# Optimization experiments

Measured on AMD Instinct MI355X. Metric: run time of the kernel, lower is better.

The kernel has to match this reference:

```python
import jax, jax.numpy as jnp
import numpy as np

N = 100_000      # nodes
E = 1_600_000    # edges
NG = 512         # graphs in batch
EPS = 1e-5


def _prop(x, src, dst, n, add_self_loops):
    """GCN-normalized sparse propagation: agg_i = sum_{j->i} d_j^-1/2 d_i^-1/2 x_j."""
    ones = jnp.ones(src.shape[0], x.dtype)
    deg = jax.ops.segment_sum(ones, dst, num_segments=n)
    if add_self_loops:
        deg = deg + 1.0
    dinv = jnp.where(deg > 0, jax.lax.rsqrt(jnp.maximum(deg, 1e-12)), 0.0)
    w = dinv[src] * dinv[dst]                       # [E]
    agg = jax.ops.segment_sum(x[src] * w[:, None], dst, num_segments=n)
    if add_self_loops:
        agg = agg + x * (dinv * dinv)[:, None]
    return agg


def setup_inputs() -> dict:
    key = jax.random.key(0)
    ks = jax.random.split(key, 24)
    w = lambda k, s: jax.random.normal(k, s, jnp.float32) * 0.05
    dim = 100
    return {
        "x": jax.random.normal(ks[0], (N, 128), jnp.float32),
        "src": jax.random.randint(ks[1], (E,), 0, N),
        "dst": jax.random.randint(ks[2], (E,), 0, N),
        "batch": jnp.sort(jax.random.randint(ks[3], (N,), 0, NG)),
        # SGConv 1 & 2 (propagate then Linear)
        "W1": w(ks[4], (128, dim)), "b1": jnp.zeros((dim,), jnp.float32),
        "W2": w(ks[5], (dim, dim)), "b2": jnp.zeros((dim,), jnp.float32),
        # BatchNorm1d affine params
        "gamma": jnp.ones((dim,), jnp.float32), "beta": jnp.zeros((dim,), jnp.float32),
        # ARMAConv (num_stacks=1, num_layers=1)
        "Wa_init": w(ks[6], (dim, dim)), "Wa_root": w(ks[7], (dim, dim)),
        "ba": jnp.zeros((dim,), jnp.float32),
        # MLP head
        "Wf1": w(ks[8], (dim, 2 * dim)), "bf1": jnp.zeros((2 * dim,), jnp.float32),
        "Wf2": w(ks[9], (2 * dim, 3 * dim)), "bf2": jnp.zeros((3 * dim,), jnp.float32),
        "Wf3": w(ks[10], (3 * dim, 2 * dim)), "bf3": jnp.zeros((2 * dim,), jnp.float32),
        "Wf4": w(ks[11], (2 * dim, 1)), "bf4": jnp.zeros((1,), jnp.float32),
    }


def reference(x, src, dst, batch, W1, b1, W2, b2, gamma, beta,
              Wa_init, Wa_root, ba, Wf1, bf1, Wf2, bf2, Wf3, bf3, Wf4, bf4):
    n = x.shape[0]
    # SGConv (K=1): propagate with self-loop gcn_norm, then linear; ReLU
    h = jax.nn.relu(_prop(x, src, dst, n, True) @ W1 + b1)
    h = jax.nn.relu(_prop(h, src, dst, n, True) @ W2 + b2)
    # BatchNorm1d (training mode: batch statistics, biased var)
    mu = jnp.mean(h, axis=0)
    var = jnp.mean((h - mu) ** 2, axis=0)
    h = (h - mu) * jax.lax.rsqrt(var + EPS) * gamma + beta
    # ARMAConv (1 stack, 1 layer): ReLU(A_hat (h W_init) + h W_root + b), no self-loops
    a = jax.nn.relu(_prop(h @ Wa_init, src, dst, n, False) + h @ Wa_root + ba)
    # global_add_pool over graph ids
    g = jax.ops.segment_sum(a, batch, num_segments=NG)   # [NG, dim]
    # MLP head
    g = jax.nn.relu(g @ Wf1 + bf1)
    g = jax.nn.relu(g @ Wf2 + bf2)
    g = jax.nn.relu(g @ Wf3 + bf3)
    return g @ Wf4 + bf4
```

## Files before the change

kernel.cpp:

```cpp
#include <hip/hip_runtime.h>
#include <hip/hip_fp16.h>

#define NNODES 100000
#define NEDGES 1600000
#define NGRAPH 512
#define DIM    100
#define DP     128
#define EPSBN  1e-5f
#define NBUK   ((NNODES + 255) >> 8)
#define BINCH  8192

typedef _Float16 half8 __attribute__((ext_vector_type(8)));
typedef float floatx4 __attribute__((ext_vector_type(4)));

__global__ __launch_bounds__(256) void bin_count_kernel(const int* __restrict__ dst,
                                                        int* __restrict__ btotal, int e) {
    __shared__ int lc[NBUK];
    int tid = threadIdx.x;
    int base = blockIdx.x * BINCH;
    int m = e - base; if (m > BINCH) m = BINCH;
    for (int b = tid; b < NBUK; b += 256) lc[b] = 0;
    __syncthreads();
    for (int j = tid; j < m; j += 256)
        atomicAdd(&lc[dst[base + j] >> 8], 1);
    __syncthreads();
    for (int b = tid; b < NBUK; b += 256)
        if (lc[b]) atomicAdd(&btotal[b], lc[b]);
}

__global__ void bucket_scan_kernel(const int* __restrict__ btotal, int* __restrict__ bbase,
                                   int* __restrict__ bcursor, int e) {
    __shared__ int s[512];
    int tid = threadIdx.x;
    int v = (tid < NBUK) ? btotal[tid] : 0;
    s[tid] = v; __syncthreads();
    for (int o = 1; o < 512; o <<= 1) {
        int t = (tid >= o) ? s[tid - o] : 0;
        __syncthreads();
        s[tid] += t;
        __syncthreads();
    }
    if (tid < NBUK) {
        int base = s[tid] - v;
        bbase[tid] = base;
        bcursor[tid] = base;
    }
    if (tid == 0) bbase[NBUK] = e;
}

__global__ __launch_bounds__(256) void bin_kernel(
        const int* __restrict__ src, const int* __restrict__ dst,
        int* __restrict__ bcursor, int2* __restrict__ gpairs, int e) {
    __shared__ int2 lpairs[BINCH];
    __shared__ int lcount[NBUK], lstart[NBUK], lcur[NBUK], gbase[NBUK];
    int tid = threadIdx.x;
    int base = blockIdx.x * BINCH;
    int m = e - base; if (m > BINCH) m = BINCH;

    for (int b = tid; b < NBUK; b += 256) lcount[b] = 0;
    __syncthreads();
    for (int j = tid; j < m; j += 256)
        atomicAdd(&lcount[dst[base + j] >> 8], 1);
    __syncthreads();
    if (tid == 0) {
        int acc = 0;
        for (int b = 0; b < NBUK; b++) {
            lstart[b] = acc;
            lcur[b] = acc;
            acc += lcount[b];
        }
    }
    __syncthreads();
    for (int b = tid; b < NBUK; b += 256)
        gbase[b] = atomicAdd(&bcursor[b], lcount[b]);
    for (int j = tid; j < m; j += 256) {
        int s = src[base + j], d = dst[base + j];
        int p = atomicAdd(&lcur[d >> 8], 1);
        lpairs[p] = make_int2(s, d);
    }
    __syncthreads();
    for (int j = tid; j < m; j += 256) {
        int2 pr = lpairs[j];
        int b = pr.y >> 8;
        gpairs[gbase[b] + (j - lstart[b])] = pr;
    }
}

__global__ __launch_bounds__(256) void bucket_build_kernel(
        const int2* __restrict__ gpairs, const int* __restrict__ bbase,
        int* __restrict__ off, int* __restrict__ ssorted,
        float* __restrict__ dsl, float* __restrict__ dnsl, int n, int e) {
    __shared__ int cnt[256];
    __shared__ int sc[256];
    int b = blockIdx.x, tid = threadIdx.x;
    int node0 = b << 8;
    int e0 = bbase[b], e1 = bbase[b + 1];

    cnt[tid] = 0;
    __syncthreads();
    for (int j = e0 + tid; j < e1; j += 256)
        atomicAdd(&cnt[gpairs[j].y & 255], 1);
    __syncthreads();

    int c = cnt[tid];
    sc[tid] = c; __syncthreads();
    for (int o = 1; o < 256; o <<= 1) {
        int t = (tid >= o) ? sc[tid - o] : 0;
        __syncthreads();
        sc[tid] += t;
        __syncthreads();
    }
    int excl = sc[tid] - c;

    int node = node0 + tid;
    if (node < n) {
        off[node] = e0 + excl;
        float cf = (float)c;
        dsl[node] = rsqrtf(cf + 1.0f);
        dnsl[node] = (c > 0) ? rsqrtf(cf) : 0.0f;
    }
    if (b == NBUK - 1 && tid == 0) off[n] = e;

    __syncthreads();
    cnt[tid] = e0 + excl;
    __syncthreads();
    for (int j = e0 + tid; j < e1; j += 256) {
        int2 pr = gpairs[j];
        int p = atomicAdd(&cnt[pr.y & 255], 1);
        ssorted[p] = pr.x;
    }
}

__global__ void packW4_kernel(const float* __restrict__ W1, const float* __restrict__ W2,
                              const float* __restrict__ W3, const float* __restrict__ W4,
                              _Float16* __restrict__ Wt1, _Float16* __restrict__ Wt2,
                              _Float16* __restrict__ Wt3, _Float16* __restrict__ Wt4) {
    int which = blockIdx.x >> 6;
    int idx = (blockIdx.x & 63) * 256 + threadIdx.x;
    const float* W = (which == 0) ? W1 : (which == 1) ? W2 : (which == 2) ? W3 : W4;
    _Float16* Wt  = (which == 0) ? Wt1 : (which == 1) ? Wt2 : (which == 2) ? Wt3 : Wt4;
    int K = (which == 0) ? 128 : DIM;
    int j = idx & 7;
    int l = (idx >> 3) & 63;
    int c = idx >> 9;
    int t = c >> 2, k0 = c & 3;
    int nn = t * 16 + (l & 15);
    int k = k0 * 32 + (l >> 4) * 8 + j;
    float v = (k < K && nn < DIM) ? W[k * DIM + nn] : 0.f;
    Wt[idx] = (_Float16)v;
}

__global__ void padb_kernel(const float* __restrict__ b1, const float* __restrict__ b2,
                            float* __restrict__ b1p, float* __restrict__ b2p) {
    int c = threadIdx.x;
    b1p[c] = (c < DIM) ? b1[c] : 0.f;
    b2p[c] = (c < DIM) ? b2[c] : 0.f;
}

__global__ __launch_bounds__(256) void prop_kernel(
        const __half* __restrict__ pre, const int* __restrict__ ssorted,
        const int* __restrict__ off, const float* __restrict__ dinv,
        const float* __restrict__ bias, __half* __restrict__ outH, int n) {
    int wave = (blockIdx.x * blockDim.x + threadIdx.x) >> 6;
    int lane = threadIdx.x & 63;
    if (wave >= n) return;
    int e0 = off[wave], e1 = off[wave + 1];
    int deg = e1 - e0;
    int g = lane >> 4;
    int q = lane & 15;

    float acc[8];
#pragma unroll
    for (int i = 0; i < 8; i++) acc[i] = 0.f;

    auto addu = [&](uint4 u) {
        float2 f;
        f = __half22float2(*(__half2*)&u.x); acc[0] += f.x; acc[1] += f.y;
        f = __half22float2(*(__half2*)&u.y); acc[2] += f.x; acc[3] += f.y;
        f = __half22float2(*(__half2*)&u.z); acc[4] += f.x; acc[5] += f.y;
        f = __half22float2(*(__half2*)&u.w); acc[6] += f.x; acc[7] += f.y;
    };
    auto rowptr = [&](int s) -> const uint4* {
        return (const uint4*)&pre[(long)s * DP + q * 8];
    };

    for (int base = 0; base < deg; base += 64) {
        int m = deg - base; if (m > 64) m = 64;
        int sidx = (lane < m) ? ssorted[e0 + base + lane] : 0;
        int j = 0;
        for (; j + 16 <= m; j += 16) {
            int s0 = __shfl(sidx, j + g);
            int s1 = __shfl(sidx, j + 4 + g);
            int s2 = __shfl(sidx, j + 8 + g);
            int s3 = __shfl(sidx, j + 12 + g);
            uint4 u0 = *rowptr(s0);
            uint4 u1 = *rowptr(s1);
            uint4 u2 = *rowptr(s2);
            uint4 u3 = *rowptr(s3);
            addu(u0); addu(u1); addu(u2); addu(u3);
        }
        for (; j + 4 <= m; j += 4) {
            int s = __shfl(sidx, j + g);
            addu(*rowptr(s));
        }
        if (j < m) {
            int r = m - j;
            int s = __shfl(sidx, (g < r) ? j + g : j);
            if (g < r) addu(*rowptr(s));
        }
    }

#pragma unroll
    for (int i = 0; i < 8; i++) {
        acc[i] += __shfl_xor(acc[i], 16);
        acc[i] += __shfl_xor(acc[i], 32);
    }

    if (g == 0) {
        float dn = dinv[wave];
        addu(*rowptr(wave));
        float4 b0 = *(const float4*)&bias[q * 8];
        float4 b1v = *(const float4*)&bias[q * 8 + 4];
        float o[8];
        o[0] = fmaxf(dn * acc[0] + b0.x, 0.f);
        o[1] = fmaxf(dn * acc[1] + b0.y, 0.f);
        o[2] = fmaxf(dn * acc[2] + b0.z, 0.f);
        o[3] = fmaxf(dn * acc[3] + b0.w, 0.f);
        o[4] = fmaxf(dn * acc[4] + b1v.x, 0.f);
        o[5] = fmaxf(dn * acc[5] + b1v.y, 0.f);
        o[6] = fmaxf(dn * acc[6] + b1v.z, 0.f);
        o[7] = fmaxf(dn * acc[7] + b1v.w, 0.f);
        __half2 p0 = __floats2half2_rn(o[0], o[1]);
        __half2 p1 = __floats2half2_rn(o[2], o[3]);
        __half2 p2 = __floats2half2_rn(o[4], o[5]);
        __half2 p3 = __floats2half2_rn(o[6], o[7]);
        uint4 u;
        u.x = *(unsigned int*)&p0;
        u.y = *(unsigned int*)&p1;
        u.z = *(unsigned int*)&p2;
        u.w = *(unsigned int*)&p3;
        *(uint4*)&outH[(long)wave * DP + q * 8] = u;
    }
}

__global__ __launch_bounds__(256) void prop_arma_kernel(
        const __half* __restrict__ pre, const int* __restrict__ ssorted,
        const int* __restrict__ off, const float* __restrict__ dinv,
        const __half* __restrict__ R, __half* __restrict__ outH, int n) {
    int wave = (blockIdx.x * blockDim.x + threadIdx.x) >> 6;
    int lane = threadIdx.x & 63;
    if (wave >= n) return;
    int e0 = off[wave], e1 = off[wave + 1];
    int deg = e1 - e0;
    int g = lane >> 4;
    int q = lane & 15;

    float acc[8];
#pragma unroll
    for (int i = 0; i < 8; i++) acc[i] = 0.f;

    auto addu = [&](uint4 u) {
        float2 f;
        f = __half22float2(*(__half2*)&u.x); acc[0] += f.x; acc[1] += f.y;
        f = __half22float2(*(__half2*)&u.y); acc[2] += f.x; acc[3] += f.y;
        f = __half22float2(*(__half2*)&u.z); acc[4] += f.x; acc[5] += f.y;
        f = __half22float2(*(__half2*)&u.w); acc[6] += f.x; acc[7] += f.y;
    };
    auto rowptr = [&](int s) -> const uint4* {
        return (const uint4*)&pre[(long)s * DP + q * 8];
    };

    for (int base = 0; base < deg; base += 64) {
        int m = deg - base; if (m > 64) m = 64;
        int sidx = (lane < m) ? ssorted[e0 + base + lane] : 0;
        int j = 0;
        for (; j + 16 <= m; j += 16) {
            int s0 = __shfl(sidx, j + g);
            int s1 = __shfl(sidx, j + 4 + g);
            int s2 = __shfl(sidx, j + 8 + g);
            int s3 = __shfl(sidx, j + 12 + g);
            uint4 u0 = *rowptr(s0);
            uint4 u1 = *rowptr(s1);
            uint4 u2 = *rowptr(s2);
            uint4 u3 = *rowptr(s3);
            addu(u0); addu(u1); addu(u2); addu(u3);
        }
        for (; j + 4 <= m; j += 4) {
            int s = __shfl(sidx, j + g);
            addu(*rowptr(s));
        }
        if (j < m) {
            int r = m - j;
            int s = __shfl(sidx, (g < r) ? j + g : j);
            if (g < r) addu(*rowptr(s));
        }
    }

#pragma unroll
    for (int i = 0; i < 8; i++) {
        acc[i] += __shfl_xor(acc[i], 16);
        acc[i] += __shfl_xor(acc[i], 32);
    }

    if (g == 0) {
        float dn = dinv[wave];
        uint4 r4 = *(const uint4*)&R[(long)wave * DP + q * 8];
        float rr[8];
        float2 f;
        f = __half22float2(*(__half2*)&r4.x); rr[0] = f.x; rr[1] = f.y;
        f = __half22float2(*(__half2*)&r4.y); rr[2] = f.x; rr[3] = f.y;
        f = __half22float2(*(__half2*)&r4.z); rr[4] = f.x; rr[5] = f.y;
        f = __half22float2(*(__half2*)&r4.w); rr[6] = f.x; rr[7] = f.y;
        float o[8];
#pragma unroll
        for (int i = 0; i < 8; i++) o[i] = fmaxf(dn * acc[i] + rr[i], 0.f);
        __half2 p0 = __floats2half2_rn(o[0], o[1]);
        __half2 p1 = __floats2half2_rn(o[2], o[3]);
        __half2 p2 = __floats2half2_rn(o[4], o[5]);
        __half2 p3 = __floats2half2_rn(o[6], o[7]);
        uint4 u;
        u.x = *(unsigned int*)&p0;
        u.y = *(unsigned int*)&p1;
        u.z = *(unsigned int*)&p2;
        u.w = *(unsigned int*)&p3;
        *(uint4*)&outH[(long)wave * DP + q * 8] = u;
    }
}

__global__ __launch_bounds__(256) void matmul_a32_kernel(
        const float* __restrict__ A, const _Float16* __restrict__ WtF,
        const float* __restrict__ rowscale, __half* __restrict__ Ch, int M) {
    __shared__ char smraw[64 * 132 * 4];
    _Float16* Bs = (_Float16*)smraw;
    float* Ct = (float*)smraw;
    int tid = threadIdx.x;
    int wave = tid >> 6;
    int lane = tid & 63;
    int m16 = lane & 15;
    int quad = lane >> 4;
    long row0blk = (long)blockIdx.x * 64;
    long row0 = row0blk + wave * 16;

    {
        const uint4* s = (const uint4*)WtF;
        uint4* d = (uint4*)Bs;
        for (int i = tid; i < 2048; i += 256) d[i] = s[i];
    }

    half8 af[4];
    {
        long ar = row0 + m16; if (ar >= M) ar = M - 1;
        const float* Ap = &A[ar * DP + quad * 8];
#pragma unroll
        for (int k0 = 0; k0 < 4; k0++) {
            float4 v0 = *(const float4*)(Ap + k0 * 32);
            float4 v1 = *(const float4*)(Ap + k0 * 32 + 4);
            half8 o;
            o[0] = (_Float16)v0.x; o[1] = (_Float16)v0.y;
            o[2] = (_Float16)v0.z; o[3] = (_Float16)v0.w;
            o[4] = (_Float16)v1.x; o[5] = (_Float16)v1.y;
            o[6] = (_Float16)v1.z; o[7] = (_Float16)v1.w;
            af[k0] = o;
        }
    }
    __syncthreads();

    floatx4 acc[8];
#pragma unroll
    for (int t = 0; t < 8; t++) acc[t] = (floatx4){0.f, 0.f, 0.f, 0.f};

#pragma unroll
    for (int c = 0; c < 32; c++) {
        half8 bf = *(const half8*)&Bs[(c * 64 + lane) * 8];
        acc[c >> 2] = __builtin_amdgcn_mfma_f32_16x16x32_f16(af[c & 3], bf, acc[c >> 2], 0, 0, 0);
    }
    __syncthreads();

    int lrow0 = wave * 16 + quad * 4;
#pragma unroll
    for (int t = 0; t < 8; t++)
#pragma unroll
        for (int r = 0; r < 4; r++)
            Ct[(lrow0 + r) * 132 + t * 16 + m16] = acc[t][r];
    __syncthreads();

    for (int idx = tid; idx < 64 * 32; idx += 256) {
        int lr = idx >> 5, c4 = idx & 31;
        long grow = row0blk + lr;
        if (grow >= M) continue;
        int col = c4 * 4;
        float4 v = *(const float4*)&Ct[lr * 132 + col];
        float rs = rowscale[grow];
        v.x *= rs; v.y *= rs; v.z *= rs; v.w *= rs;
        __half2 p01 = __floats2half2_rn(v.x, v.y);
        __half2 p23 = __floats2half2_rn(v.z, v.w);
        uint2 u;
        u.x = *(unsigned int*)&p01;
        u.y = *(unsigned int*)&p23;
        *(uint2*)&Ch[grow * DP + col] = u;
    }
}

__global__ __launch_bounds__(256) void matmul_a16_kernel(
        const __half* __restrict__ A, const _Float16* __restrict__ WtF,
        const float* __restrict__ rowscale, __half* __restrict__ Ch, int M) {
    __shared__ char smraw[64 * 132 * 4];
    _Float16* Bs = (_Float16*)smraw;
    float* Ct = (float*)smraw;
    int tid = threadIdx.x;
    int wave = tid >> 6;
    int lane = tid & 63;
    int m16 = lane & 15;
    int quad = lane >> 4;
    long row0blk = (long)blockIdx.x * 64;
    long row0 = row0blk + wave * 16;

    {
        const uint4* s = (const uint4*)WtF;
        uint4* d = (uint4*)Bs;
        for (int i = tid; i < 2048; i += 256) d[i] = s[i];
    }

    half8 af[4];
    {
        long ar = row0 + m16; if (ar >= M) ar = M - 1;
        const _Float16* Ap = (const _Float16*)&A[ar * DP + quad * 8];
#pragma unroll
        for (int k0 = 0; k0 < 4; k0++)
            af[k0] = *(const half8*)(Ap + k0 * 32);
    }
    __syncthreads();

    floatx4 acc[8];
#pragma unroll
    for (int t = 0; t < 8; t++) acc[t] = (floatx4){0.f, 0.f, 0.f, 0.f};

#pragma unroll
    for (int c = 0; c < 32; c++) {
        half8 bf = *(const half8*)&Bs[(c * 64 + lane) * 8];
        acc[c >> 2] = __builtin_amdgcn_mfma_f32_16x16x32_f16(af[c & 3], bf, acc[c >> 2], 0, 0, 0);
    }
    __syncthreads();

    int lrow0 = wave * 16 + quad * 4;
#pragma unroll
    for (int t = 0; t < 8; t++)
#pragma unroll
        for (int r = 0; r < 4; r++)
            Ct[(lrow0 + r) * 132 + t * 16 + m16] = acc[t][r];
    __syncthreads();

    for (int idx = tid; idx < 64 * 32; idx += 256) {
        int lr = idx >> 5, c4 = idx & 31;
        long grow = row0blk + lr;
        if (grow >= M) continue;
        int col = c4 * 4;
        float4 v = *(const float4*)&Ct[lr * 132 + col];
        float rs = rowscale[grow];
        v.x *= rs; v.y *= rs; v.z *= rs; v.w *= rs;
        __half2 p01 = __floats2half2_rn(v.x, v.y);
        __half2 p23 = __floats2half2_rn(v.z, v.w);
        uint2 u;
        u.x = *(unsigned int*)&p01;
        u.y = *(unsigned int*)&p23;
        *(uint2*)&Ch[grow * DP + col] = u;
    }
}

__global__ __launch_bounds__(256) void matmul_dual_kernel(
        const __half* __restrict__ A, const _Float16* __restrict__ WtF3,
        const _Float16* __restrict__ WtF4, const float* __restrict__ ba,
        const float* __restrict__ rowscale,
        const float* __restrict__ bnscale, const float* __restrict__ bnshift,
        __half* __restrict__ Ch1, __half* __restrict__ ChR, int M, int Kout) {
    __shared__ char smraw[64 * 132 * 4];
    _Float16* Bs = (_Float16*)smraw;
    float* Ct = (float*)smraw;
    int tid = threadIdx.x;
    int wave = tid >> 6;
    int lane = tid & 63;
    int m16 = lane & 15;
    int quad = lane >> 4;
    long row0blk = (long)blockIdx.x * 64;
    long row0 = row0blk + wave * 16;

    half8 af[4];
    {
        long ar = row0 + m16; if (ar >= M) ar = M - 1;
        const _Float16* Ap = (const _Float16*)&A[ar * DP + quad * 8];
#pragma unroll
        for (int k0 = 0; k0 < 4; k0++) {
            half8 h = *(const half8*)(Ap + k0 * 32);
            int c0 = quad * 8 + k0 * 32;
            float4 sc0 = *(const float4*)&bnscale[c0];
            float4 sc1 = *(const float4*)&bnscale[c0 + 4];
            float4 sh0 = *(const float4*)&bnshift[c0];
            float4 sh1 = *(const float4*)&bnshift[c0 + 4];
            half8 o;
            o[0] = (_Float16)((float)h[0] * sc0.x + sh0.x);
            o[1] = (_Float16)((float)h[1] * sc0.y + sh0.y);
            o[2] = (_Float16)((float)h[2] * sc0.z + sh0.z);
            o[3] = (_Float16)((float)h[3] * sc0.w + sh0.w);
            o[4] = (_Float16)((float)h[4] * sc1.x + sh1.x);
            o[5] = (_Float16)((float)h[5] * sc1.y + sh1.y);
            o[6] = (_Float16)((float)h[6] * sc1.z + sh1.z);
            o[7] = (_Float16)((float)h[7] * sc1.w + sh1.w);
            af[k0] = o;
        }
    }

    floatx4 acc3[8], acc4[8];
#pragma unroll
    for (int t = 0; t < 8; t++) {
        acc3[t] = (floatx4){0.f, 0.f, 0.f, 0.f};
        acc4[t] = (floatx4){0.f, 0.f, 0.f, 0.f};
    }

    {
        const uint4* s = (const uint4*)WtF3;
        uint4* d = (uint4*)Bs;
        for (int i = tid; i < 2048; i += 256) d[i] = s[i];
    }
    __syncthreads();
#pragma unroll
    for (int c = 0; c < 32; c++) {
        half8 bf = *(const half8*)&Bs[(c * 64 + lane) * 8];
        acc3[c >> 2] = __builtin_amdgcn_mfma_f32_16x16x32_f16(af[c & 3], bf, acc3[c >> 2], 0, 0, 0);
    }
    __syncthreads();

    {
        const uint4* s = (const uint4*)WtF4;
        uint4* d = (uint4*)Bs;
        for (int i = tid; i < 2048; i += 256) d[i] = s[i];
    }
    __syncthreads();
#pragma unroll
    for (int c = 0; c < 32; c++) {
        half8 bf = *(const half8*)&Bs[(c * 64 + lane) * 8];
        acc4[c >> 2] = __builtin_amdgcn_mfma_f32_16x16x32_f16(af[c & 3], bf, acc4[c >> 2], 0, 0, 0);
    }
    __syncthreads();

    int lrow0 = wave * 16 + quad * 4;

#pragma unroll
    for (int t = 0; t < 8; t++)
#pragma unroll
        for (int r = 0; r < 4; r++)
            Ct[(lrow0 + r) * 132 + t * 16 + m16] = acc3[t][r];
    __syncthreads();
    for (int idx = tid; idx < 64 * 32; idx += 256) {
        int lr = idx >> 5, c4 = idx & 31;
        long grow = row0blk + lr;
        if (grow >= M) continue;
        int col = c4 * 4;
        float4 v = *(const float4*)&Ct[lr * 132 + col];
        float rs = rowscale[grow];
        v.x *= rs; v.y *= rs; v.z *= rs; v.w *= rs;
        __half2 p01 = __floats2half2_rn(v.x, v.y);
        __half2 p23 = __floats2half2_rn(v.z, v.w);
        uint2 u;
        u.x = *(unsigned int*)&p01;
        u.y = *(unsigned int*)&p23;
        *(uint2*)&Ch1[grow * DP + col] = u;
    }
    __syncthreads();

#pragma unroll
    for (int t = 0; t < 8; t++)
#pragma unroll
        for (int r = 0; r < 4; r++)
            Ct[(lrow0 + r) * 132 + t * 16 + m16] = acc4[t][r];
    __syncthreads();
    for (int idx = tid; idx < 64 * 32; idx += 256) {
        int lr = idx >> 5, c4 = idx & 31;
        long grow = row0blk + lr;
        if (grow >= M) continue;
        int col = c4 * 4;
        float4 v = *(const float4*)&Ct[lr * 132 + col];
        if (col + 4 <= Kout) {
            float4 bb = *(const float4*)&ba[col];
            v.x += bb.x; v.y += bb.y; v.z += bb.z; v.w += bb.w;
        }
        __half2 p01 = __floats2half2_rn(v.x, v.y);
        __half2 p23 = __floats2half2_rn(v.z, v.w);
        uint2 u;
        u.x = *(unsigned int*)&p01;
        u.y = *(unsigned int*)&p23;
        *(uint2*)&ChR[grow * DP + col] = u;
    }
}

__global__ __launch_bounds__(512) void bnstats_kernel(const __half* __restrict__ h,
                                                      float* __restrict__ bnsum,
                                                      float* __restrict__ bnsq, int n) {
    __shared__ float2 sred[512], qred[512];
    int tid = threadIdx.x;
    int col2 = tid & 63;
    int rgrp = tid >> 6;
    float2 s = make_float2(0.f, 0.f), qv = make_float2(0.f, 0.f);
    if (col2 < 52) {
        for (int r = blockIdx.x * 8 + rgrp; r < n; r += gridDim.x * 8) {
            __half2 hv = *(const __half2*)&h[(long)r * DP + col2 * 2];
            float2 f = __half22float2(hv);
            s.x += f.x; s.y += f.y;
            qv.x += f.x * f.x; qv.y += f.y * f.y;
        }
    }
    sred[tid] = s; qred[tid] = qv;
    __syncthreads();
    if (tid < 52) {
        float2 ts = make_float2(0.f, 0.f), tq = make_float2(0.f, 0.f);
#pragma unroll
        for (int gg = 0; gg < 8; gg++) {
            float2 v = sred[gg * 64 + tid]; ts.x += v.x; ts.y += v.y;
            v = qred[gg * 64 + tid]; tq.x += v.x; tq.y += v.y;
        }
        atomicAdd(&bnsum[tid * 2], ts.x);
        atomicAdd(&bnsum[tid * 2 + 1], ts.y);
        atomicAdd(&bnsq[tid * 2], tq.x);
        atomicAdd(&bnsq[tid * 2 + 1], tq.y);
    }
}

__global__ void bn_prep_kernel(const float* __restrict__ sum, const float* __restrict__ sq,
                               const float* __restrict__ gamma, const float* __restrict__ beta,
                               float* __restrict__ scale, float* __restrict__ shift, int n) {
    int c = threadIdx.x;
    float sc = 0.f, sh = 0.f;
    if (c < DIM) {
        float inv_n = 1.0f / (float)n;
        float mu = sum[c] * inv_n;
        float var = sq[c] * inv_n - mu * mu;
        float rs = rsqrtf(var + EPSBN);
        sc = rs * gamma[c];
        sh = beta[c] - mu * sc;
    }
    scale[c] = sc;
    shift[c] = sh;
}

__global__ void gbounds_kernel(const int* __restrict__ batch, int* __restrict__ gstart, int n) {
    int g = threadIdx.x;
    int lo = 0, hi = n;
    while (lo < hi) {
        int mid = (lo + hi) >> 1;
        if (batch[mid] < g) lo = mid + 1; else hi = mid;
    }
    gstart[g] = lo;
    if (g == 0) gstart[NGRAPH] = n;
}

__global__ __launch_bounds__(512) void pool_kernel(const __half* __restrict__ a,
                                                   const int* __restrict__ gstart,
                                                   float* __restrict__ g) {
    __shared__ float2 red[512];
    int b = blockIdx.x, tid = threadIdx.x;
    int col2 = tid & 63;
    int rgrp = tid >> 6;
    int lo = gstart[b], hi = gstart[b + 1];
    float2 s = make_float2(0.f, 0.f);
    for (int r = lo + rgrp; r < hi; r += 8) {
        __half2 h = *(const __half2*)&a[(long)r * DP + col2 * 2];
        float2 f = __half22float2(h);
        s.x += f.x; s.y += f.y;
    }
    red[tid] = s;
    __syncthreads();
    if (tid < 64) {
        float2 t = make_float2(0.f, 0.f);
#pragma unroll
        for (int gg = 0; gg < 8; gg++) {
            float2 v = red[gg * 64 + tid];
            t.x += v.x; t.y += v.y;
        }
        *(float2*)&g[b * DP + tid * 2] = t;
    }
}

__global__ __launch_bounds__(256) void mlp_kernel(
        const float* __restrict__ g,
        const float* __restrict__ Wf1, const float* __restrict__ bf1,
        const float* __restrict__ Wf2, const float* __restrict__ bf2,
        const float* __restrict__ Wf3, const float* __restrict__ bf3,
        const float* __restrict__ Wf4, const float* __restrict__ bf4,
        float* __restrict__ out) {
    __shared__ float a0[100], a1[200], a2[300], a3[200], red[256];
    int b = blockIdx.x, tid = threadIdx.x;
    if (tid < 100) a0[tid] = g[b * DP + tid];
    __syncthreads();
    for (int c = tid; c < 200; c += 256) {
        float s = bf1[c];
        for (int k = 0; k < 100; k++) s += a0[k] * Wf1[k * 200 + c];
        a1[c] = fmaxf(s, 0.f);
    }
    __syncthreads();
    for (int c = tid; c < 300; c += 256) {
        float s = bf2[c];
        for (int k = 0; k < 200; k++) s += a1[k] * Wf2[k * 300 + c];
        a2[c] = fmaxf(s, 0.f);
    }
    __syncthreads();
    for (int c = tid; c < 200; c += 256) {
        float s = bf3[c];
        for (int k = 0; k < 300; k++) s += a2[k] * Wf3[k * 200 + c];
        a3[c] = fmaxf(s, 0.f);
    }
    __syncthreads();
    red[tid] = (tid < 200) ? a3[tid] * Wf4[tid] : 0.f;
    __syncthreads();
    for (int o = 128; o > 0; o >>= 1) {
        if (tid < o) red[tid] += red[tid + o];
        __syncthreads();
    }
    if (tid == 0) out[b] = red[0] + bf4[0];
}

extern "C" void kernel_launch(void* const* d_in, const int* in_sizes, int n_in,
                              void* d_out, int out_size, void* d_ws, size_t ws_size,
                              hipStream_t stream) {
    const float* x      = (const float*)d_in[0];
    const int*   src    = (const int*)d_in[1];
    const int*   dst    = (const int*)d_in[2];
    const int*   batch  = (const int*)d_in[3];
    const float* W1     = (const float*)d_in[4];
    const float* b1     = (const float*)d_in[5];
    const float* W2     = (const float*)d_in[6];
    const float* b2     = (const float*)d_in[7];
    const float* gamma  = (const float*)d_in[8];
    const float* beta   = (const float*)d_in[9];
    const float* Wa_init= (const float*)d_in[10];
    const float* Wa_root= (const float*)d_in[11];
    const float* ba     = (const float*)d_in[12];
    const float* Wf1    = (const float*)d_in[13];
    const float* bf1    = (const float*)d_in[14];
    const float* Wf2    = (const float*)d_in[15];
    const float* bf2    = (const float*)d_in[16];
    const float* Wf3    = (const float*)d_in[17];
    const float* bf3    = (const float*)d_in[18];
    const float* Wf4    = (const float*)d_in[19];
    const float* bf4    = (const float*)d_in[20];
    float* out = (float*)d_out;

    const int n = NNODES;
    const int e = NEDGES;

    char* ws = (char*)d_ws;
    auto carve = [&](size_t bytes) -> void* {
        void* p = (void*)ws;
        ws += (bytes + 255) & ~(size_t)255;
        return p;
    };
    __half* buf0    = (__half*)carve((size_t)n * DP * 2);
    __half* buf1    = (__half*)carve((size_t)n * DP * 2);
    __half* bufR    = (__half*)carve((size_t)n * DP * 2);
    __half* bufC    = (__half*)carve((size_t)n * DP * 2);
    _Float16* Wt1   = (_Float16*)carve((size_t)DP * DP * 2);
    _Float16* Wt2   = (_Float16*)carve((size_t)DP * DP * 2);
    _Float16* Wt3   = (_Float16*)carve((size_t)DP * DP * 2);
    _Float16* Wt4   = (_Float16*)carve((size_t)DP * DP * 2);
    int*    off     = (int*)carve((size_t)(n + 1) * 4);
    int*    btotal  = (int*)carve((size_t)NBUK * 4);
    int*    bbase   = (int*)carve((size_t)(NBUK + 1) * 4);
    int*    bcursor = (int*)carve((size_t)NBUK * 4);
    int*    ssorted = (int*)carve((size_t)e * 4);
    int2*   gpairs  = (int2*)carve((size_t)e * 8);
    float*  dinv_sl = (float*)carve((size_t)n * 4);
    float*  dinv_nsl= (float*)carve((size_t)n * 4);
    float*  bnsum   = (float*)carve(DP * 4);
    float*  bnsq    = (float*)carve(DP * 4);
    float*  bnscale = (float*)carve(DP * 4);
    float*  bnshift = (float*)carve(DP * 4);
    float*  b1p     = (float*)carve(DP * 4);
    float*  b2p     = (float*)carve(DP * 4);
    int*    gstart  = (int*)carve((size_t)(NGRAPH + 1) * 4);
    float*  gpool   = (float*)carve((size_t)NGRAPH * DP * 4);

    const int nchunk = (e + BINCH - 1) / BINCH;

    packW4_kernel<<<256, 256, 0, stream>>>(W1, W2, Wa_init, Wa_root, Wt1, Wt2, Wt3, Wt4);
    padb_kernel<<<1, 128, 0, stream>>>(b1, b2, b1p, b2p);

    hipMemsetAsync(btotal, 0, (size_t)NBUK * 4, stream);
    hipMemsetAsync(bnsum, 0, DP * 4, stream);
    hipMemsetAsync(bnsq, 0, DP * 4, stream);
    bin_count_kernel<<<nchunk, 256, 0, stream>>>(dst, btotal, e);
    bucket_scan_kernel<<<1, 512, 0, stream>>>(btotal, bbase, bcursor, e);
    bin_kernel<<<nchunk, 256, 0, stream>>>(src, dst, bcursor, gpairs, e);
    bucket_build_kernel<<<NBUK, 256, 0, stream>>>(gpairs, bbase, off, ssorted, dinv_sl, dinv_nsl, n, e);
    gbounds_kernel<<<1, 512, 0, stream>>>(batch, gstart, n);

    const int prop_blocks = (n + 3) / 4;
    const int mm_blocks = (n + 63) / 64;

    matmul_a32_kernel<<<mm_blocks, 256, 0, stream>>>(x, Wt1, dinv_sl, buf0, n);
    prop_kernel<<<prop_blocks, 256, 0, stream>>>(buf0, ssorted, off, dinv_sl, b1p, buf1, n);

    matmul_a16_kernel<<<mm_blocks, 256, 0, stream>>>(buf1, Wt2, dinv_sl, buf0, n);
    prop_kernel<<<prop_blocks, 256, 0, stream>>>(buf0, ssorted, off, dinv_sl, b2p, buf1, n);

    bnstats_kernel<<<512, 512, 0, stream>>>(buf1, bnsum, bnsq, n);
    bn_prep_kernel<<<1, 128, 0, stream>>>(bnsum, bnsq, gamma, beta, bnscale, bnshift, n);

    matmul_dual_kernel<<<mm_blocks, 256, 0, stream>>>(buf1, Wt3, Wt4, ba, dinv_nsl, bnscale, bnshift, buf0, bufR, n, DIM);
    prop_arma_kernel<<<prop_blocks, 256, 0, stream>>>(buf0, ssorted, off, dinv_nsl, bufR, bufC, n);

    pool_kernel<<<NGRAPH, 512, 0, stream>>>(bufC, gstart, gpool);

    mlp_kernel<<<NGRAPH, 256, 0, stream>>>(gpool, Wf1, bf1, Wf2, bf2, Wf3, bf3, Wf4, bf4, out);
}
```

Measured before the change: 532.1 us.

## Fuse small setup kernels, pack edge pairs, pad gather loop with zero row

Merges the bias padding and the memsets into the weight-pack kernel, folds the graph-bounds search into the bucket scan, and fuses pooling with the MLP head, all to cut launch count. Edge pairs are packed into 32-bit words (src<<8 | local dst), which halves the bin traffic. The prop loops now always run in 16-edge steps, and missing lanes point at a zeroed extra row appended to buf0. That removes the tail branches at the cost of some wasted loads. The packing assumes src fits in 24 bits, and the zero row only works for prop inputs that read from buf0.

```diff
diff --git a/kernel.cpp b/kernel.cpp
--- a/kernel.cpp
+++ b/kernel.cpp
@@ -29,7 +29,8 @@
 }
 
 __global__ void bucket_scan_kernel(const int* __restrict__ btotal, int* __restrict__ bbase,
-                                   int* __restrict__ bcursor, int e) {
+                                   int* __restrict__ bcursor, int e,
+                                   const int* __restrict__ batch, int* __restrict__ gstart, int n) {
     __shared__ int s[512];
     int tid = threadIdx.x;
     int v = (tid < NBUK) ? btotal[tid] : 0;
@@ -46,11 +47,22 @@
         bcursor[tid] = base;
     }
     if (tid == 0) bbase[NBUK] = e;
+
+    {
+        int g = tid;
+        int lo = 0, hi = n;
+        while (lo < hi) {
+            int mid = (lo + hi) >> 1;
+            if (batch[mid] < g) lo = mid + 1; else hi = mid;
+        }
+        gstart[g] = lo;
+        if (g == 0) gstart[NGRAPH] = n;
+    }
 }
 
 __global__ __launch_bounds__(256) void bin_kernel(
         const int* __restrict__ src, const int* __restrict__ dst,
-        int* __restrict__ bcursor, int2* __restrict__ gpairs, int e) {
+        int* __restrict__ bcursor, unsigned int* __restrict__ gpairs, int e) {
     __shared__ int2 lpairs[BINCH];
     __shared__ int lcount[NBUK], lstart[NBUK], lcur[NBUK], gbase[NBUK];
     int tid = threadIdx.x;
@@ -82,12 +94,13 @@
     for (int j = tid; j < m; j += 256) {
         int2 pr = lpairs[j];
         int b = pr.y >> 8;
-        gpairs[gbase[b] + (j - lstart[b])] = pr;
+        gpairs[gbase[b] + (j - lstart[b])] =
+            ((unsigned int)pr.x << 8) | ((unsigned int)pr.y & 255u);
     }
 }
 
 __global__ __launch_bounds__(256) void bucket_build_kernel(
-        const int2* __restrict__ gpairs, const int* __restrict__ bbase,
+        const unsigned int* __restrict__ gpairs, const int* __restrict__ bbase,
         int* __restrict__ off, int* __restrict__ ssorted,
         float* __restrict__ dsl, float* __restrict__ dnsl, int n, int e) {
     __shared__ int cnt[256];
@@ -99,7 +112,7 @@
     cnt[tid] = 0;
     __syncthreads();
     for (int j = e0 + tid; j < e1; j += 256)
-        atomicAdd(&cnt[gpairs[j].y & 255], 1);
+        atomicAdd(&cnt[gpairs[j] & 255u], 1);
     __syncthreads();
 
     int c = cnt[tid];
@@ -125,16 +138,32 @@
     cnt[tid] = e0 + excl;
     __syncthreads();
     for (int j = e0 + tid; j < e1; j += 256) {
-        int2 pr = gpairs[j];
-        int p = atomicAdd(&cnt[pr.y & 255], 1);
-        ssorted[p] = pr.x;
+        unsigned int pk = gpairs[j];
+        int p = atomicAdd(&cnt[pk & 255u], 1);
+        ssorted[p] = (int)(pk >> 8);
     }
 }
 
 __global__ void packW4_kernel(const float* __restrict__ W1, const float* __restrict__ W2,
                               const float* __restrict__ W3, const float* __restrict__ W4,
                               _Float16* __restrict__ Wt1, _Float16* __restrict__ Wt2,
-                              _Float16* __restrict__ Wt3, _Float16* __restrict__ Wt4) {
+                              _Float16* __restrict__ Wt3, _Float16* __restrict__ Wt4,
+                              const float* __restrict__ b1, const float* __restrict__ b2,
+                              float* __restrict__ b1p, float* __restrict__ b2p,
+                              int* __restrict__ btotal, float* __restrict__ bnsum,
+                              float* __restrict__ bnsq, __half* __restrict__ buf0zr) {
+    if (blockIdx.x == 256) {
+        int t = threadIdx.x;
+        if (t < 128) {
+            b1p[t] = (t < DIM) ? b1[t] : 0.f;
+            b2p[t] = (t < DIM) ? b2[t] : 0.f;
+            bnsum[t] = 0.f;
+            bnsq[t] = 0.f;
+        }
+        for (int i = t; i < NBUK; i += 256) btotal[i] = 0;
+        if (t < 64) ((unsigned int*)buf0zr)[t] = 0u;
+        return;
+    }
     int which = blockIdx.x >> 6;
     int idx = (blockIdx.x & 63) * 256 + threadIdx.x;
     const float* W = (which == 0) ? W1 : (which == 1) ? W2 : (which == 2) ? W3 : W4;
@@ -150,13 +179,6 @@
     Wt[idx] = (_Float16)v;
 }
 
-__global__ void padb_kernel(const float* __restrict__ b1, const float* __restrict__ b2,
-                            float* __restrict__ b1p, float* __restrict__ b2p) {
-    int c = threadIdx.x;
-    b1p[c] = (c < DIM) ? b1[c] : 0.f;
-    b2p[c] = (c < DIM) ? b2[c] : 0.f;
-}
-
 __global__ __launch_bounds__(256) void prop_kernel(
         const __half* __restrict__ pre, const int* __restrict__ ssorted,
         const int* __restrict__ off, const float* __restrict__ dinv,
@@ -168,6 +190,7 @@
     int deg = e1 - e0;
     int g = lane >> 4;
     int q = lane & 15;
+    const int ZR = n;
 
     float acc[8];
 #pragma unroll
@@ -186,9 +209,8 @@
 
     for (int base = 0; base < deg; base += 64) {
         int m = deg - base; if (m > 64) m = 64;
-        int sidx = (lane < m) ? ssorted[e0 + base + lane] : 0;
-        int j = 0;
-        for (; j + 16 <= m; j += 16) {
+        int sidx = (lane < m) ? ssorted[e0 + base + lane] : ZR;
+        for (int j = 0; j < m; j += 16) {
             int s0 = __shfl(sidx, j + g);
             int s1 = __shfl(sidx, j + 4 + g);
             int s2 = __shfl(sidx, j + 8 + g);
@@ -198,15 +220,6 @@
             uint4 u2 = *rowptr(s2);
             uint4 u3 = *rowptr(s3);
             addu(u0); addu(u1); addu(u2); addu(u3);
-        }
-        for (; j + 4 <= m; j += 4) {
-            int s = __shfl(sidx, j + g);
-            addu(*rowptr(s));
-        }
-        if (j < m) {
-            int r = m - j;
-            int s = __shfl(sidx, (g < r) ? j + g : j);
-            if (g < r) addu(*rowptr(s));
         }
     }
 
@@ -254,6 +267,7 @@
     int deg = e1 - e0;
     int g = lane >> 4;
     int q = lane & 15;
+    const int ZR = n;
 
     float acc[8];
 #pragma unroll
@@ -272,9 +286,8 @@
 
     for (int base = 0; base < deg; base += 64) {
         int m = deg - base; if (m > 64) m = 64;
-        int sidx = (lane < m) ? ssorted[e0 + base + lane] : 0;
-        int j = 0;
-        for (; j + 16 <= m; j += 16) {
+        int sidx = (lane < m) ? ssorted[e0 + base + lane] : ZR;
+        for (int j = 0; j < m; j += 16) {
             int s0 = __shfl(sidx, j + g);
             int s1 = __shfl(sidx, j + 4 + g);
             int s2 = __shfl(sidx, j + 8 + g);
@@ -284,15 +297,6 @@
             uint4 u2 = *rowptr(s2);
             uint4 u3 = *rowptr(s3);
             addu(u0); addu(u1); addu(u2); addu(u3);
-        }
-        for (; j + 4 <= m; j += 4) {
-            int s = __shfl(sidx, j + g);
-            addu(*rowptr(s));
-        }
-        if (j < m) {
-            int r = m - j;
-            int s = __shfl(sidx, (g < r) ? j + g : j);
-            if (g < r) addu(*rowptr(s));
         }
     }
 
@@ -641,80 +645,67 @@
     shift[c] = sh;
 }
 
-__global__ void gbounds_kernel(const int* __restrict__ batch, int* __restrict__ gstart, int n) {
-    int g = threadIdx.x;
-    int lo = 0, hi = n;
-    while (lo < hi) {
-        int mid = (lo + hi) >> 1;
-        if (batch[mid] < g) lo = mid + 1; else hi = mid;
-    }
-    gstart[g] = lo;
-    if (g == 0) gstart[NGRAPH] = n;
-}
-
-__global__ __launch_bounds__(512) void pool_kernel(const __half* __restrict__ a,
-                                                   const int* __restrict__ gstart,
-                                                   float* __restrict__ g) {
-    __shared__ float2 red[512];
-    int b = blockIdx.x, tid = threadIdx.x;
-    int col2 = tid & 63;
-    int rgrp = tid >> 6;
-    int lo = gstart[b], hi = gstart[b + 1];
-    float2 s = make_float2(0.f, 0.f);
-    for (int r = lo + rgrp; r < hi; r += 8) {
-        __half2 h = *(const __half2*)&a[(long)r * DP + col2 * 2];
-        float2 f = __half22float2(h);
-        s.x += f.x; s.y += f.y;
-    }
-    red[tid] = s;
-    __syncthreads();
-    if (tid < 64) {
-        float2 t = make_float2(0.f, 0.f);
-#pragma unroll
-        for (int gg = 0; gg < 8; gg++) {
-            float2 v = red[gg * 64 + tid];
-            t.x += v.x; t.y += v.y;
-        }
-        *(float2*)&g[b * DP + tid * 2] = t;
-    }
-}
-
-__global__ __launch_bounds__(256) void mlp_kernel(
-        const float* __restrict__ g,
+__global__ __launch_bounds__(512) void pmlp_kernel(
+        const __half* __restrict__ a, const int* __restrict__ gstart,
         const float* __restrict__ Wf1, const float* __restrict__ bf1,
         const float* __restrict__ Wf2, const float* __restrict__ bf2,
         const float* __restrict__ Wf3, const float* __restrict__ bf3,
         const float* __restrict__ Wf4, const float* __restrict__ bf4,
         float* __restrict__ out) {
-    __shared__ float a0[100], a1[200], a2[300], a3[200], red[256];
+    __shared__ float2 red[512];
+    __shared__ float gsum[128], a1[200], a2[300], a3[200], red1[512];
     int b = blockIdx.x, tid = threadIdx.x;
-    if (tid < 100) a0[tid] = g[b * DP + tid];
-    __syncthreads();
-    for (int c = tid; c < 200; c += 256) {
+
+    {
+        int col2 = tid & 63;
+        int rgrp = tid >> 6;
+        int lo = gstart[b], hi = gstart[b + 1];
+        float2 s = make_float2(0.f, 0.f);
+        for (int r = lo + rgrp; r < hi; r += 8) {
+            __half2 h = *(const __half2*)&a[(long)r * DP + col2 * 2];
+            float2 f = __half22float2(h);
+            s.x += f.x; s.y += f.y;
+        }
+        red[tid] = s;
+        __syncthreads();
+        if (tid < 64) {
+            float2 t = make_float2(0.f, 0.f);
+#pragma unroll
+            for (int gg = 0; gg < 8; gg++) {
+                float2 v = red[gg * 64 + tid];
+                t.x += v.x; t.y += v.y;
+            }
+            gsum[tid * 2] = t.x;
+            gsum[tid * 2 + 1] = t.y;
+        }
+        __syncthreads();
+    }
+
+    for (int c = tid; c < 200; c += 512) {
         float s = bf1[c];
-        for (int k = 0; k < 100; k++) s += a0[k] * Wf1[k * 200 + c];
+        for (int k = 0; k < 100; k++) s += gsum[k] * Wf1[k * 200 + c];
         a1[c] = fmaxf(s, 0.f);
     }
     __syncthreads();
-    for (int c = tid; c < 300; c += 256) {
+    for (int c = tid; c < 300; c += 512) {
         float s = bf2[c];
         for (int k = 0; k < 200; k++) s += a1[k] * Wf2[k * 300 + c];
         a2[c] = fmaxf(s, 0.f);
     }
     __syncthreads();
-    for (int c = tid; c < 200; c += 256) {
+    for (int c = tid; c < 200; c += 512) {
         float s = bf3[c];
         for (int k = 0; k < 300; k++) s += a2[k] * Wf3[k * 200 + c];
         a3[c] = fmaxf(s, 0.f);
     }
     __syncthreads();
-    red[tid] = (tid < 200) ? a3[tid] * Wf4[tid] : 0.f;
-    __syncthreads();
-    for (int o = 128; o > 0; o >>= 1) {
-        if (tid < o) red[tid] += red[tid + o];
+    red1[tid] = (tid < 200) ? a3[tid] * Wf4[tid] : 0.f;
+    __syncthreads();
+    for (int o = 256; o > 0; o >>= 1) {
+        if (tid < o) red1[tid] += red1[tid + o];
         __syncthreads();
     }
-    if (tid == 0) out[b] = red[0] + bf4[0];
+    if (tid == 0) out[b] = red1[0] + bf4[0];
 }
 
 extern "C" void kernel_launch(void* const* d_in, const int* in_sizes, int n_in,
@@ -752,7 +743,7 @@
         ws += (bytes + 255) & ~(size_t)255;
         return p;
     };
-    __half* buf0    = (__half*)carve((size_t)n * DP * 2);
+    __half* buf0    = (__half*)carve((size_t)(n + 1) * DP * 2);
     __half* buf1    = (__half*)carve((size_t)n * DP * 2);
     __half* bufR    = (__half*)carve((size_t)n * DP * 2);
     __half* bufC    = (__half*)carve((size_t)n * DP * 2);
@@ -765,7 +756,7 @@
     int*    bbase   = (int*)carve((size_t)(NBUK + 1) * 4);
     int*    bcursor = (int*)carve((size_t)NBUK * 4);
     int*    ssorted = (int*)carve((size_t)e * 4);
-    int2*   gpairs  = (int2*)carve((size_t)e * 8);
+    unsigned int* gpairs = (unsigned int*)carve((size_t)e * 4);
     float*  dinv_sl = (float*)carve((size_t)n * 4);
     float*  dinv_nsl= (float*)carve((size_t)n * 4);
     float*  bnsum   = (float*)carve(DP * 4);
@@ -775,21 +766,17 @@
     float*  b1p     = (float*)carve(DP * 4);
     float*  b2p     = (float*)carve(DP * 4);
     int*    gstart  = (int*)carve((size_t)(NGRAPH + 1) * 4);
-    float*  gpool   = (float*)carve((size_t)NGRAPH * DP * 4);
 
     const int nchunk = (e + BINCH - 1) / BINCH;
 
-    packW4_kernel<<<256, 256, 0, stream>>>(W1, W2, Wa_init, Wa_root, Wt1, Wt2, Wt3, Wt4);
-    padb_kernel<<<1, 128, 0, stream>>>(b1, b2, b1p, b2p);
-
-    hipMemsetAsync(btotal, 0, (size_t)NBUK * 4, stream);
-    hipMemsetAsync(bnsum, 0, DP * 4, stream);
-    hipMemsetAsync(bnsq, 0, DP * 4, stream);
+    packW4_kernel<<<257, 256, 0, stream>>>(W1, W2, Wa_init, Wa_root, Wt1, Wt2, Wt3, Wt4,
+                                           b1, b2, b1p, b2p, btotal, bnsum, bnsq,
+                                           buf0 + (size_t)n * DP);
+
     bin_count_kernel<<<nchunk, 256, 0, stream>>>(dst, btotal, e);
-    bucket_scan_kernel<<<1, 512, 0, stream>>>(btotal, bbase, bcursor, e);
+    bucket_scan_kernel<<<1, 512, 0, stream>>>(btotal, bbase, bcursor, e, batch, gstart, n);
     bin_kernel<<<nchunk, 256, 0, stream>>>(src, dst, bcursor, gpairs, e);
     bucket_build_kernel<<<NBUK, 256, 0, stream>>>(gpairs, bbase, off, ssorted, dinv_sl, dinv_nsl, n, e);
-    gbounds_kernel<<<1, 512, 0, stream>>>(batch, gstart, n);
 
     const int prop_blocks = (n + 3) / 4;
     const int mm_blocks = (n + 63) / 64;
@@ -806,7 +793,5 @@
     matmul_dual_kernel<<<mm_blocks, 256, 0, stream>>>(buf1, Wt3, Wt4, ba, dinv_nsl, bnscale, bnshift, buf0, bufR, n, DIM);
     prop_arma_kernel<<<prop_blocks, 256, 0, stream>>>(buf0, ssorted, off, dinv_nsl, bufR, bufC, n);
 
-    pool_kernel<<<NGRAPH, 512, 0, stream>>>(bufC, gstart, gpool);
-
-    mlp_kernel<<<NGRAPH, 256, 0, stream>>>(gpool, Wf1, bf1, Wf2, bf2, Wf3, bf3, Wf4, bf4, out);
-}
+    pmlp_kernel<<<NGRAPH, 512, 0, stream>>>(bufC, gstart, Wf1, bf1, Wf2, bf2, Wf3, bf3, Wf4, bf4, out);
+}
```

Result: faster. 503.3 us (-5.4%).
